# Kernel tuning notes

Measured on AMD Instinct MI355X. Metric: run time of the kernel, lower is better.

## Reference

```python
import jax, jax.numpy as jnp
import numpy as np

N_NODES = 100000
N_EDGES = 1600000
IN_FEATS = 128
OUT_FEATS = 128
LN_EPS = 1e-5


def setup_inputs() -> dict:
    key = jax.random.key(0)
    k_h, k_w, k_b, k_src, k_dst = jax.random.split(key, 5)
    stdv = 1.0 / np.sqrt(OUT_FEATS)
    return {
        "h": jax.random.normal(k_h, (N_NODES, IN_FEATS), dtype=jnp.float32),
        "weight": jax.random.uniform(k_w, (IN_FEATS, OUT_FEATS), dtype=jnp.float32, minval=-stdv, maxval=stdv),
        "bias": jax.random.uniform(k_b, (OUT_FEATS,), dtype=jnp.float32, minval=-stdv, maxval=stdv),
        "gamma": jnp.ones((OUT_FEATS,), dtype=jnp.float32),
        "beta": jnp.zeros((OUT_FEATS,), dtype=jnp.float32),
        "src": jax.random.randint(k_src, (N_EDGES,), 0, N_NODES, dtype=jnp.int32),
        "dst": jax.random.randint(k_dst, (N_EDGES,), 0, N_NODES, dtype=jnp.int32),
    }


def reference(h, weight, bias, gamma, beta, src, dst):
    n = h.shape[0]
    # in-degree norm: 1/deg with inf -> 0 (isolated nodes)
    deg = jax.ops.segment_sum(jnp.ones_like(dst, dtype=h.dtype), dst, num_segments=n)
    norm = jnp.where(deg > 0, 1.0 / deg, 0.0)[:, None]  # [N, 1]
    # update_all(copy_src, sum): scatter-add of source features onto destinations
    ah = jax.ops.segment_sum(h[src], dst, num_segments=n)  # [N, in_feats]
    x = ah * norm
    x = x @ weight + bias  # [N, out_feats]
    # LayerNorm over feature dim with affine params
    mu = jnp.mean(x, axis=-1, keepdims=True)
    var = jnp.mean(jnp.square(x - mu), axis=-1, keepdims=True)
    x = (x - mu) * jax.lax.rsqrt(var + LN_EPS) * gamma + beta
    return jax.nn.relu(x)
```

## Files before the change

kernel.cpp:

```cpp
#include <hip/hip_runtime.h>

#define F 128
#define SCANB 1024
#define NBLK 128
#define BSHIFT 6
#define MAXNB 4096
#define SMEM_BYTES 43264

typedef __attribute__((ext_vector_type(8))) short short8;
typedef __attribute__((ext_vector_type(4))) float f32x4;

static __device__ __forceinline__ short f2bf(float f) {
    union { float f; unsigned u; } v; v.f = f;
    unsigned r = v.u + 0x7FFF + ((v.u >> 16) & 1);
    return (short)(r >> 16);
}
static __device__ __forceinline__ float bf_lo(unsigned u) {
    return __builtin_bit_cast(float, u << 16);
}
static __device__ __forceinline__ float bf_hi(unsigned u) {
    return __builtin_bit_cast(float, u & 0xFFFF0000u);
}
static __device__ __forceinline__ uint4 pack8(float a0,float a1,float a2,float a3,
                                              float a4,float a5,float a6,float a7) {
    uint4 o;
    o.x = ((unsigned)(unsigned short)f2bf(a1) << 16) | (unsigned short)f2bf(a0);
    o.y = ((unsigned)(unsigned short)f2bf(a3) << 16) | (unsigned short)f2bf(a2);
    o.z = ((unsigned)(unsigned short)f2bf(a5) << 16) | (unsigned short)f2bf(a4);
    o.w = ((unsigned)(unsigned short)f2bf(a7) << 16) | (unsigned short)f2bf(a6);
    return o;
}

__global__ __launch_bounds__(256) void k_gemm_hist(
    const float* __restrict__ h, const float* __restrict__ w,
    unsigned* __restrict__ hb, const int* __restrict__ dst,
    int* __restrict__ mat, int n_nodes, int n_edges, int nb, int hblk) {
    __shared__ alignas(16) char smem[SMEM_BYTES];
    const int tid = threadIdx.x;
    const int bid = blockIdx.x;

    if (bid < hblk) {
        int* lh = (int*)smem;
        for (int i = tid; i < nb; i += 256) lh[i] = 0;
        __syncthreads();
        const int epb = (n_edges + hblk - 1) / hblk;
        const int e0 = bid * epb, e1 = min(e0 + epb, n_edges);
        for (int e = e0 + tid; e < e1; e += 256)
            atomicAdd(&lh[dst[e] >> BSHIFT], 1);
        __syncthreads();
        for (int i = tid; i < nb; i += 256)
            mat[(size_t)i * NBLK + bid] = lh[i];
        return;
    }

    short* wt = (short*)smem;
    float* xs = (float*)(smem + 34816);
    {
        int n = tid & 127;
        for (int k = tid >> 7; k < 128; k += 2)
            wt[n * 136 + k] = f2bf(w[(size_t)k * 128 + n]);
    }
    __syncthreads();

    const int wv = tid >> 6, l = tid & 63, lr = l & 15, lk = l >> 4, q = l & 15;
    const int base = (bid - hblk) * 64;
    if (base >= n_nodes) return;
    const int row = base + wv * 16 + lr;
    const bool valid = row < n_nodes;

    short8 af[4];
    #pragma unroll
    for (int kk = 0; kk < 4; ++kk) {
        int k0 = kk * 32 + lk * 8;
        float4 a0{0,0,0,0}, a1{0,0,0,0};
        if (valid) {
            a0 = *(const float4*)(h + (size_t)row * F + k0);
            a1 = *(const float4*)(h + (size_t)row * F + k0 + 4);
        }
        af[kk] = short8{ f2bf(a0.x), f2bf(a0.y), f2bf(a0.z), f2bf(a0.w),
                         f2bf(a1.x), f2bf(a1.y), f2bf(a1.z), f2bf(a1.w) };
    }
    f32x4 acc[8];
    #pragma unroll
    for (int n = 0; n < 8; ++n) acc[n] = f32x4{0, 0, 0, 0};
    #pragma unroll
    for (int kk = 0; kk < 4; ++kk) {
        const int kb = kk * 32 + lk * 8;
        #pragma unroll
        for (int n = 0; n < 8; ++n) {
            short8 bfr = *(const short8*)(&wt[(n * 16 + lr) * 136 + kb]);
            acc[n] = __builtin_amdgcn_mfma_f32_16x16x32_bf16(af[kk], bfr, acc[n], 0, 0, 0);
        }
    }
    float* xw = xs + wv * (4 * 132);
    #pragma unroll
    for (int r = 0; r < 4; ++r) {
        #pragma unroll
        for (int n = 0; n < 8; ++n)
            xw[lk * 132 + n * 16 + lr] = acc[n][r];
        int grow = base + wv * 16 + lk * 4 + r;
        float4 a = *(const float4*)&xw[lk * 132 + q * 8];
        float4 b = *(const float4*)&xw[lk * 132 + q * 8 + 4];
        uint4 o = pack8(a.x, a.y, a.z, a.w, b.x, b.y, b.z, b.w);
        if (grow < n_nodes)
            ((uint4*)hb)[(size_t)grow * 16 + q] = o;
    }
}

__global__ __launch_bounds__(SCANB) void k_scan_a(const int* in, int* out,
                                                  int* bsum, int n) {
    __shared__ int tmp[SCANB];
    int i = blockIdx.x * SCANB + threadIdx.x;
    int v = (i < n) ? in[i] : 0;
    tmp[threadIdx.x] = v;
    __syncthreads();
    for (int off = 1; off < SCANB; off <<= 1) {
        int t = (threadIdx.x >= off) ? tmp[threadIdx.x - off] : 0;
        __syncthreads();
        tmp[threadIdx.x] += t;
        __syncthreads();
    }
    if (i < n) out[i] = tmp[threadIdx.x] - v;
    if (threadIdx.x == SCANB - 1) bsum[blockIdx.x] = tmp[SCANB - 1];
}

__global__ __launch_bounds__(512) void k_scan_b(int* bsum, int nb) {
    __shared__ int tmp[512];
    int i = threadIdx.x;
    int v = (i < nb) ? bsum[i] : 0;
    tmp[i] = v;
    __syncthreads();
    for (int off = 1; off < 512; off <<= 1) {
        int t = (i >= off) ? tmp[i - off] : 0;
        __syncthreads();
        tmp[i] += t;
        __syncthreads();
    }
    if (i < nb) bsum[i] = tmp[i] - v;
}

__global__ __launch_bounds__(SCANB) void k_scan_c(int* out, const int* bsum, int n) {
    int i = blockIdx.x * SCANB + threadIdx.x;
    if (i < n) out[i] += bsum[blockIdx.x];
}

__global__ __launch_bounds__(256) void k_part_scatter(
    const int* __restrict__ src, const int* __restrict__ dst,
    const int* __restrict__ mat, const int* __restrict__ bsum,
    unsigned* __restrict__ binned, int n_edges, int nb, int epb) {
    __shared__ int lbase[MAXNB];
    const int bid = blockIdx.x;
    for (int i = threadIdx.x; i < nb; i += 256) {
        int idx = i * NBLK + bid;
        lbase[i] = mat[idx] + bsum[idx >> 10];
    }
    __syncthreads();
    int e0 = bid * epb;
    int e1 = min(e0 + epb, n_edges);
    for (int e = e0 + threadIdx.x; e < e1; e += 256) {
        int d = dst[e];
        int b = d >> BSHIFT;
        int pos = atomicAdd(&lbase[b], 1);
        binned[pos] = ((unsigned)(d & ((1 << BSHIFT) - 1)) << 26) | (unsigned)src[e];
    }
}

__global__ __launch_bounds__(256) void k_bin_to_csr(
    const unsigned* __restrict__ binned, const int* __restrict__ mat,
    const int* __restrict__ bsum, int* __restrict__ deg, int* __restrict__ offs,
    int* __restrict__ esrc, int n_edges, int n_nodes, int nb) {
    __shared__ int ldeg[64], loffs[64], lcur[64];
    int b = blockIdx.x;
    int i0 = b * NBLK;
    int start = mat[i0] + bsum[i0 >> 10];
    int end = n_edges;
    if (b + 1 < nb) {
        int i1 = (b + 1) * NBLK;
        end = mat[i1] + bsum[i1 >> 10];
    }
    int cnt = end - start;
    int base_node = b << BSHIFT;
    int nn = min(1 << BSHIFT, n_nodes - base_node);
    for (int i = threadIdx.x; i < nn; i += 256) { ldeg[i] = 0; lcur[i] = 0; }
    __syncthreads();
    for (int i = threadIdx.x; i < cnt; i += 256)
        atomicAdd(&ldeg[binned[start + i] >> 26], 1);
    __syncthreads();
    if (threadIdx.x == 0) {
        int run = 0;
        for (int i = 0; i < nn; ++i) { loffs[i] = run; run += ldeg[i]; }
    }
    __syncthreads();
    for (int i = threadIdx.x; i < nn; i += 256) {
        deg[base_node + i]  = ldeg[i];
        offs[base_node + i] = start + loffs[i];
    }
    for (int i = threadIdx.x; i < cnt; i += 256) {
        unsigned p = binned[start + i];
        int ln = p >> 26;
        int pos = start + loffs[ln] + atomicAdd(&lcur[ln], 1);
        esrc[pos] = (int)(p & ((1u << 26) - 1));
    }
}

__global__ __launch_bounds__(256) void k_hist(const int* __restrict__ dst,
                                              int* __restrict__ deg, int n_edges) {
    int e = blockIdx.x * 256 + threadIdx.x;
    if (e < n_edges) atomicAdd(&deg[dst[e]], 1);
}

__global__ __launch_bounds__(256) void k_scatter_idx(
    const int* __restrict__ src, const int* __restrict__ dst,
    const int* __restrict__ offs, int* __restrict__ cursor,
    int* __restrict__ esrc, int n_edges) {
    int e = blockIdx.x * 256 + threadIdx.x;
    if (e >= n_edges) return;
    int d = dst[e];
    int pos = offs[d] + atomicAdd(&cursor[d], 1);
    esrc[pos] = src[e];
}

__global__ __launch_bounds__(256) void k_gather_ln(
    const unsigned* __restrict__ hb, const int* __restrict__ esrc,
    const int* __restrict__ offs, const int* __restrict__ deg,
    const float* __restrict__ bias, const float* __restrict__ gamma,
    const float* __restrict__ beta, float* __restrict__ out, int n_nodes) {
    int t = blockIdx.x * 256 + threadIdx.x;
    int node = t >> 6;
    int l = t & 63;
    if (node >= n_nodes) return;
    const int g = l >> 4;
    const int q = l & 15;

    float4 bs0 = *(const float4*)(bias  + q * 8);
    float4 bs1 = *(const float4*)(bias  + q * 8 + 4);
    float4 gm0 = *(const float4*)(gamma + q * 8);
    float4 gm1 = *(const float4*)(gamma + q * 8 + 4);
    float4 bt0 = *(const float4*)(beta  + q * 8);
    float4 bt1 = *(const float4*)(beta  + q * 8 + 4);

    const int start = offs[node];
    const int dn = deg[node];
    const int end = start + dn;

    float a0=0,a1=0,a2=0,a3=0,a4=0,a5=0,a6=0,a7=0;
    int i = start;
    for (; i + 8 <= end; i += 8) {
        int s0 = esrc[i + g];
        int s1 = esrc[i + 4 + g];
        uint4 v0 = *((const uint4*)(hb + (size_t)s0 * 64 + q * 4));
        uint4 v1 = *((const uint4*)(hb + (size_t)s1 * 64 + q * 4));
        a0 += bf_lo(v0.x) + bf_lo(v1.x); a1 += bf_hi(v0.x) + bf_hi(v1.x);
        a2 += bf_lo(v0.y) + bf_lo(v1.y); a3 += bf_hi(v0.y) + bf_hi(v1.y);
        a4 += bf_lo(v0.z) + bf_lo(v1.z); a5 += bf_hi(v0.z) + bf_hi(v1.z);
        a6 += bf_lo(v0.w) + bf_lo(v1.w); a7 += bf_hi(v0.w) + bf_hi(v1.w);
    }
    for (; i < end; i += 4) {
        int e = i + g;
        if (e < end) {
            int s = esrc[e];
            uint4 v = *((const uint4*)(hb + (size_t)s * 64 + q * 4));
            a0 += bf_lo(v.x); a1 += bf_hi(v.x);
            a2 += bf_lo(v.y); a3 += bf_hi(v.y);
            a4 += bf_lo(v.z); a5 += bf_hi(v.z);
            a6 += bf_lo(v.w); a7 += bf_hi(v.w);
        }
    }
    #pragma unroll
    for (int m = 16; m <= 32; m <<= 1) {
        a0 += __shfl_xor(a0, m); a1 += __shfl_xor(a1, m);
        a2 += __shfl_xor(a2, m); a3 += __shfl_xor(a3, m);
        a4 += __shfl_xor(a4, m); a5 += __shfl_xor(a5, m);
        a6 += __shfl_xor(a6, m); a7 += __shfl_xor(a7, m);
    }
    const float nv = dn > 0 ? 1.0f / (float)dn : 0.0f;
    float f0 = a0 * nv + bs0.x, f1 = a1 * nv + bs0.y;
    float f2 = a2 * nv + bs0.z, f3 = a3 * nv + bs0.w;
    float f4 = a4 * nv + bs1.x, f5 = a5 * nv + bs1.y;
    float f6 = a6 * nv + bs1.z, f7 = a7 * nv + bs1.w;

    float s  = ((f0 + f1) + (f2 + f3)) + ((f4 + f5) + (f6 + f7));
    float q2 = ((f0*f0 + f1*f1) + (f2*f2 + f3*f3)) + ((f4*f4 + f5*f5) + (f6*f6 + f7*f7));
    #pragma unroll
    for (int m = 1; m <= 8; m <<= 1) {
        s  += __shfl_xor(s, m);
        q2 += __shfl_xor(q2, m);
    }
    float mu   = s * (1.0f / F);
    float var  = q2 * (1.0f / F) - mu * mu;
    float rstd = rsqrtf(var + 1e-5f);

    if (g == 0) {
        float4 o0, o1;
        o0.x = fmaxf((f0 - mu) * rstd * gm0.x + bt0.x, 0.0f);
        o0.y = fmaxf((f1 - mu) * rstd * gm0.y + bt0.y, 0.0f);
        o0.z = fmaxf((f2 - mu) * rstd * gm0.z + bt0.z, 0.0f);
        o0.w = fmaxf((f3 - mu) * rstd * gm0.w + bt0.w, 0.0f);
        o1.x = fmaxf((f4 - mu) * rstd * gm1.x + bt1.x, 0.0f);
        o1.y = fmaxf((f5 - mu) * rstd * gm1.y + bt1.y, 0.0f);
        o1.z = fmaxf((f6 - mu) * rstd * gm1.z + bt1.z, 0.0f);
        o1.w = fmaxf((f7 - mu) * rstd * gm1.w + bt1.w, 0.0f);
        float* op = out + (size_t)node * F + q * 8;
        *(float4*)op = o0;
        *(float4*)(op + 4) = o1;
    }
}

extern "C" void kernel_launch(void* const* d_in, const int* in_sizes, int n_in,
                              void* d_out, int out_size, void* d_ws, size_t ws_size,
                              hipStream_t stream) {
    const float* h      = (const float*)d_in[0];
    const float* weight = (const float*)d_in[1];
    const float* bias   = (const float*)d_in[2];
    const float* gamma  = (const float*)d_in[3];
    const float* beta   = (const float*)d_in[4];
    const int*   src    = (const int*)d_in[5];
    const int*   dst    = (const int*)d_in[6];

    const int n_nodes = in_sizes[0] / F;
    const int n_edges = in_sizes[5];

    float* x = (float*)d_out;

    const int nb = (n_nodes + (1 << BSHIFT) - 1) >> BSHIFT;
    const int len = nb * NBLK;
    const int nscan = (len + SCANB - 1) / SCANB;
    const bool shift_ok = (nb <= MAXNB) && (nscan <= 512) && (n_nodes <= (1 << 26));

    int* deg    = (int*)d_ws;
    int* offs   = deg + n_nodes;
    int* esrc   = offs + n_nodes;
    unsigned* hb = (unsigned*)(esrc + n_edges);
    int* bsum   = (int*)(hb + (size_t)n_nodes * 64);
    int* mat    = bsum + 1024;
    unsigned* binned = (unsigned*)(mat + (size_t)len);
    int* cursor = mat;

    size_t need_common = ((size_t)2 * n_nodes + (size_t)n_edges + 1024) * sizeof(int)
                       + (size_t)n_nodes * 64 * sizeof(unsigned);
    size_t need_new  = need_common + ((size_t)len + (size_t)n_edges) * sizeof(int);
    size_t need_fall = need_common + (size_t)n_nodes * sizeof(int);
    bool use_new = shift_ok && ws_size >= need_new;

    const int gb = (n_nodes + 63) / 64;

    if (use_new) {
        k_gemm_hist<<<NBLK + gb, 256, 0, stream>>>(h, weight, hb, dst, mat,
                                                   n_nodes, n_edges, nb, NBLK);
        k_scan_a<<<nscan, SCANB, 0, stream>>>(mat, mat, bsum, len);
        k_scan_b<<<1, 512, 0, stream>>>(bsum, nscan);
        const int epb = (n_edges + NBLK - 1) / NBLK;
        k_part_scatter<<<NBLK, 256, 0, stream>>>(src, dst, mat, bsum, binned,
                                                 n_edges, nb, epb);
        k_bin_to_csr<<<nb, 256, 0, stream>>>(binned, mat, bsum, deg, offs, esrc,
                                             n_edges, n_nodes, nb);
    } else if (ws_size >= need_fall) {
        k_gemm_hist<<<gb, 256, 0, stream>>>(h, weight, hb, dst, mat,
                                            n_nodes, n_edges, nb, 0);
        const int nscan2 = (n_nodes + SCANB - 1) / SCANB;
        hipMemsetAsync(deg, 0, (size_t)n_nodes * sizeof(int), stream);
        hipMemsetAsync(cursor, 0, (size_t)n_nodes * sizeof(int), stream);
        k_hist<<<(n_edges + 255) / 256, 256, 0, stream>>>(dst, deg, n_edges);
        k_scan_a<<<nscan2, SCANB, 0, stream>>>(deg, offs, bsum, n_nodes);
        k_scan_b<<<1, 512, 0, stream>>>(bsum, nscan2);
        k_scan_c<<<nscan2, SCANB, 0, stream>>>(offs, bsum, n_nodes);
        k_scatter_idx<<<(n_edges + 255) / 256, 256, 0, stream>>>(
            src, dst, offs, cursor, esrc, n_edges);
    }

    int gblocks = (int)(((size_t)n_nodes * 64 + 255) / 256);
    k_gather_ln<<<gblocks, 256, 0, stream>>>(hb, esrc, offs, deg,
                                             bias, gamma, beta, x, n_nodes);
}
```

Measured before the change: 144.8 us.

## Fuse bin-to-CSR conversion with gather, normalization and LayerNorm per bin

```diff
diff --git a/kernel.cpp b/kernel.cpp
--- a/kernel.cpp
+++ b/kernel.cpp
@@ -5,6 +5,7 @@
 #define NBLK 128
 #define BSHIFT 6
 #define MAXNB 4096
+#define CAP 4096
 #define SMEM_BYTES 43264
 
 typedef __attribute__((ext_vector_type(8))) short short8;
@@ -165,41 +166,134 @@
     }
 }
 
-__global__ __launch_bounds__(256) void k_bin_to_csr(
+__global__ __launch_bounds__(256) void k_csr_gather(
     const unsigned* __restrict__ binned, const int* __restrict__ mat,
-    const int* __restrict__ bsum, int* __restrict__ deg, int* __restrict__ offs,
-    int* __restrict__ esrc, int n_edges, int n_nodes, int nb) {
+    const int* __restrict__ bsum, const unsigned* __restrict__ hb,
+    const float* __restrict__ bias, const float* __restrict__ gamma,
+    const float* __restrict__ beta, int* __restrict__ esrc,
+    float* __restrict__ out, int n_edges, int n_nodes, int nb) {
     __shared__ int ldeg[64], loffs[64], lcur[64];
-    int b = blockIdx.x;
-    int i0 = b * NBLK;
-    int start = mat[i0] + bsum[i0 >> 10];
+    __shared__ int lesrc[CAP];
+
+    const int tid = threadIdx.x;
+    const int b = blockIdx.x;
+    const int i0 = b * NBLK;
+    const int start = mat[i0] + bsum[i0 >> 10];
     int end = n_edges;
     if (b + 1 < nb) {
         int i1 = (b + 1) * NBLK;
         end = mat[i1] + bsum[i1 >> 10];
     }
-    int cnt = end - start;
-    int base_node = b << BSHIFT;
-    int nn = min(1 << BSHIFT, n_nodes - base_node);
-    for (int i = threadIdx.x; i < nn; i += 256) { ldeg[i] = 0; lcur[i] = 0; }
-    __syncthreads();
-    for (int i = threadIdx.x; i < cnt; i += 256)
+    const int cnt = end - start;
+    const int base_node = b << BSHIFT;
+    const int nn = min(1 << BSHIFT, n_nodes - base_node);
+
+    for (int i = tid; i < 64; i += 256) { ldeg[i] = 0; lcur[i] = 0; }
+    __syncthreads();
+    for (int i = tid; i < cnt; i += 256)
         atomicAdd(&ldeg[binned[start + i] >> 26], 1);
     __syncthreads();
-    if (threadIdx.x == 0) {
+    if (tid == 0) {
         int run = 0;
         for (int i = 0; i < nn; ++i) { loffs[i] = run; run += ldeg[i]; }
     }
     __syncthreads();
-    for (int i = threadIdx.x; i < nn; i += 256) {
-        deg[base_node + i]  = ldeg[i];
-        offs[base_node + i] = start + loffs[i];
-    }
-    for (int i = threadIdx.x; i < cnt; i += 256) {
-        unsigned p = binned[start + i];
-        int ln = p >> 26;
-        int pos = start + loffs[ln] + atomicAdd(&lcur[ln], 1);
-        esrc[pos] = (int)(p & ((1u << 26) - 1));
+
+    const bool inLds = cnt <= CAP;
+    if (inLds) {
+        for (int i = tid; i < cnt; i += 256) {
+            unsigned p = binned[start + i];
+            int ln = p >> 26;
+            int pos = loffs[ln] + atomicAdd(&lcur[ln], 1);
+            lesrc[pos] = (int)(p & ((1u << 26) - 1));
+        }
+    } else {
+        for (int i = tid; i < cnt; i += 256) {
+            unsigned p = binned[start + i];
+            int ln = p >> 26;
+            int pos = loffs[ln] + atomicAdd(&lcur[ln], 1);
+            esrc[start + pos] = (int)(p & ((1u << 26) - 1));
+        }
+    }
+    __syncthreads();
+
+    const int wv = tid >> 6, l = tid & 63, g = l >> 4, q = l & 15;
+    const int* ep = inLds ? (const int*)lesrc : (const int*)(esrc + start);
+
+    float4 bs0 = *(const float4*)(bias  + q * 8);
+    float4 bs1 = *(const float4*)(bias  + q * 8 + 4);
+    float4 gm0 = *(const float4*)(gamma + q * 8);
+    float4 gm1 = *(const float4*)(gamma + q * 8 + 4);
+    float4 bt0 = *(const float4*)(beta  + q * 8);
+    float4 bt1 = *(const float4*)(beta  + q * 8 + 4);
+
+    for (int ni = 0; ni < 16; ++ni) {
+        int ln = wv * 16 + ni;
+        if (ln >= nn) break;
+        const int eb = loffs[ln];
+        const int dn = ldeg[ln];
+
+        float a0=0,a1=0,a2=0,a3=0,a4=0,a5=0,a6=0,a7=0;
+        int i = 0;
+        for (; i + 8 <= dn; i += 8) {
+            int s0 = ep[eb + i + g];
+            int s1 = ep[eb + i + 4 + g];
+            uint4 v0 = *((const uint4*)(hb + (size_t)s0 * 64 + q * 4));
+            uint4 v1 = *((const uint4*)(hb + (size_t)s1 * 64 + q * 4));
+            a0 += bf_lo(v0.x) + bf_lo(v1.x); a1 += bf_hi(v0.x) + bf_hi(v1.x);
+            a2 += bf_lo(v0.y) + bf_lo(v1.y); a3 += bf_hi(v0.y) + bf_hi(v1.y);
+            a4 += bf_lo(v0.z) + bf_lo(v1.z); a5 += bf_hi(v0.z) + bf_hi(v1.z);
+            a6 += bf_lo(v0.w) + bf_lo(v1.w); a7 += bf_hi(v0.w) + bf_hi(v1.w);
+        }
+        for (; i < dn; i += 4) {
+            int e = i + g;
+            if (e < dn) {
+                int s = ep[eb + e];
+                uint4 v = *((const uint4*)(hb + (size_t)s * 64 + q * 4));
+                a0 += bf_lo(v.x); a1 += bf_hi(v.x);
+                a2 += bf_lo(v.y); a3 += bf_hi(v.y);
+                a4 += bf_lo(v.z); a5 += bf_hi(v.z);
+                a6 += bf_lo(v.w); a7 += bf_hi(v.w);
+            }
+        }
+        #pragma unroll
+        for (int m = 16; m <= 32; m <<= 1) {
+            a0 += __shfl_xor(a0, m); a1 += __shfl_xor(a1, m);
+            a2 += __shfl_xor(a2, m); a3 += __shfl_xor(a3, m);
+            a4 += __shfl_xor(a4, m); a5 += __shfl_xor(a5, m);
+            a6 += __shfl_xor(a6, m); a7 += __shfl_xor(a7, m);
+        }
+        const float nv = dn > 0 ? 1.0f / (float)dn : 0.0f;
+        float f0 = a0 * nv + bs0.x, f1 = a1 * nv + bs0.y;
+        float f2 = a2 * nv + bs0.z, f3 = a3 * nv + bs0.w;
+        float f4 = a4 * nv + bs1.x, f5 = a5 * nv + bs1.y;
+        float f6 = a6 * nv + bs1.z, f7 = a7 * nv + bs1.w;
+
+        float s  = ((f0 + f1) + (f2 + f3)) + ((f4 + f5) + (f6 + f7));
+        float q2 = ((f0*f0 + f1*f1) + (f2*f2 + f3*f3)) + ((f4*f4 + f5*f5) + (f6*f6 + f7*f7));
+        #pragma unroll
+        for (int m = 1; m <= 8; m <<= 1) {
+            s  += __shfl_xor(s, m);
+            q2 += __shfl_xor(q2, m);
+        }
+        float mu   = s * (1.0f / F);
+        float var  = q2 * (1.0f / F) - mu * mu;
+        float rstd = rsqrtf(var + 1e-5f);
+
+        if (g == 0) {
+            float4 o0, o1;
+            o0.x = fmaxf((f0 - mu) * rstd * gm0.x + bt0.x, 0.0f);
+            o0.y = fmaxf((f1 - mu) * rstd * gm0.y + bt0.y, 0.0f);
+            o0.z = fmaxf((f2 - mu) * rstd * gm0.z + bt0.z, 0.0f);
+            o0.w = fmaxf((f3 - mu) * rstd * gm0.w + bt0.w, 0.0f);
+            o1.x = fmaxf((f4 - mu) * rstd * gm1.x + bt1.x, 0.0f);
+            o1.y = fmaxf((f5 - mu) * rstd * gm1.y + bt1.y, 0.0f);
+            o1.z = fmaxf((f6 - mu) * rstd * gm1.z + bt1.z, 0.0f);
+            o1.w = fmaxf((f7 - mu) * rstd * gm1.w + bt1.w, 0.0f);
+            float* op = out + (size_t)(base_node + ln) * F + q * 8;
+            *(float4*)op = o0;
+            *(float4*)(op + 4) = o1;
+        }
     }
 }
 
@@ -352,7 +446,8 @@
         const int epb = (n_edges + NBLK - 1) / NBLK;
         k_part_scatter<<<NBLK, 256, 0, stream>>>(src, dst, mat, bsum, binned,
                                                  n_edges, nb, epb);
-        k_bin_to_csr<<<nb, 256, 0, stream>>>(binned, mat, bsum, deg, offs, esrc,
+        k_csr_gather<<<nb, 256, 0, stream>>>(binned, mat, bsum, hb,
+                                             bias, gamma, beta, esrc, x,
                                              n_edges, n_nodes, nb);
     } else if (ws_size >= need_fall) {
         k_gemm_hist<<<gb, 256, 0, stream>>>(h, weight, hb, dst, mat,
@@ -366,9 +461,8 @@
         k_scan_c<<<nscan2, SCANB, 0, stream>>>(offs, bsum, n_nodes);
         k_scatter_idx<<<(n_edges + 255) / 256, 256, 0, stream>>>(
             src, dst, offs, cursor, esrc, n_edges);
-    }
-
-    int gblocks = (int)(((size_t)n_nodes * 64 + 255) / 256);
-    k_gather_ln<<<gblocks, 256, 0, stream>>>(hb, esrc, offs, deg,
-                                             bias, gamma, beta, x, n_nodes);
-}
+        int gblocks = (int)(((size_t)n_nodes * 64 + 255) / 256);
+        k_gather_ln<<<gblocks, 256, 0, stream>>>(hb, esrc, offs, deg,
+                                                 bias, gamma, beta, x, n_nodes);
+    }
+}
```

Result: slower. 155.9 us (+7.7%).

## Split GEMM tiles across histogram and scatter kernels; unroll gather by 16

Applied to the files above, without the earlier changes.

```diff
diff --git a/kernel.cpp b/kernel.cpp
--- a/kernel.cpp
+++ b/kernel.cpp
@@ -31,28 +31,9 @@
     return o;
 }
 
-__global__ __launch_bounds__(256) void k_gemm_hist(
+static __device__ __forceinline__ void gemm_tile(
     const float* __restrict__ h, const float* __restrict__ w,
-    unsigned* __restrict__ hb, const int* __restrict__ dst,
-    int* __restrict__ mat, int n_nodes, int n_edges, int nb, int hblk) {
-    __shared__ alignas(16) char smem[SMEM_BYTES];
-    const int tid = threadIdx.x;
-    const int bid = blockIdx.x;
-
-    if (bid < hblk) {
-        int* lh = (int*)smem;
-        for (int i = tid; i < nb; i += 256) lh[i] = 0;
-        __syncthreads();
-        const int epb = (n_edges + hblk - 1) / hblk;
-        const int e0 = bid * epb, e1 = min(e0 + epb, n_edges);
-        for (int e = e0 + tid; e < e1; e += 256)
-            atomicAdd(&lh[dst[e] >> BSHIFT], 1);
-        __syncthreads();
-        for (int i = tid; i < nb; i += 256)
-            mat[(size_t)i * NBLK + bid] = lh[i];
-        return;
-    }
-
+    unsigned* __restrict__ hb, int n_nodes, int base, char* smem, int tid) {
     short* wt = (short*)smem;
     float* xs = (float*)(smem + 34816);
     {
@@ -63,7 +44,6 @@
     __syncthreads();
 
     const int wv = tid >> 6, l = tid & 63, lr = l & 15, lk = l >> 4, q = l & 15;
-    const int base = (bid - hblk) * 64;
     if (base >= n_nodes) return;
     const int row = base + wv * 16 + lr;
     const bool valid = row < n_nodes;
@@ -107,6 +87,60 @@
     }
 }
 
+__global__ __launch_bounds__(256) void k_gemm_hist(
+    const float* __restrict__ h, const float* __restrict__ w,
+    unsigned* __restrict__ hb, const int* __restrict__ dst,
+    int* __restrict__ mat, int n_nodes, int n_edges, int nb, int hblk) {
+    __shared__ alignas(16) char smem[SMEM_BYTES];
+    const int tid = threadIdx.x;
+    const int bid = blockIdx.x;
+
+    if (bid < hblk) {
+        int* lh = (int*)smem;
+        for (int i = tid; i < nb; i += 256) lh[i] = 0;
+        __syncthreads();
+        const int epb = (n_edges + hblk - 1) / hblk;
+        const int e0 = bid * epb, e1 = min(e0 + epb, n_edges);
+        for (int e = e0 + tid; e < e1; e += 256)
+            atomicAdd(&lh[dst[e] >> BSHIFT], 1);
+        __syncthreads();
+        for (int i = tid; i < nb; i += 256)
+            mat[(size_t)i * NBLK + bid] = lh[i];
+        return;
+    }
+    gemm_tile(h, w, hb, n_nodes, (bid - hblk) * 64, smem, tid);
+}
+
+__global__ __launch_bounds__(256) void k_scatter_gemm(
+    const int* __restrict__ src, const int* __restrict__ dst,
+    const int* __restrict__ mat, const int* __restrict__ bsum,
+    unsigned* __restrict__ binned, int n_edges, int nb, int epb,
+    const float* __restrict__ h, const float* __restrict__ w,
+    unsigned* __restrict__ hb, int n_nodes, int row0) {
+    __shared__ alignas(16) char smem[SMEM_BYTES];
+    const int tid = threadIdx.x;
+    const int bid = blockIdx.x;
+
+    if (bid < NBLK) {
+        int* lbase = (int*)smem;
+        for (int i = tid; i < nb; i += 256) {
+            int idx = i * NBLK + bid;
+            lbase[i] = mat[idx] + bsum[idx >> 10];
+        }
+        __syncthreads();
+        int e0 = bid * epb;
+        int e1 = min(e0 + epb, n_edges);
+        for (int e = e0 + tid; e < e1; e += 256) {
+            int d = dst[e];
+            int b = d >> BSHIFT;
+            int pos = atomicAdd(&lbase[b], 1);
+            binned[pos] = ((unsigned)(d & ((1 << BSHIFT) - 1)) << 26) | (unsigned)src[e];
+        }
+        return;
+    }
+    gemm_tile(h, w, hb, n_nodes, row0 + (bid - NBLK) * 64, smem, tid);
+}
+
 __global__ __launch_bounds__(SCANB) void k_scan_a(const int* in, int* out,
                                                   int* bsum, int n) {
     __shared__ int tmp[SCANB];
@@ -142,27 +176,6 @@
 __global__ __launch_bounds__(SCANB) void k_scan_c(int* out, const int* bsum, int n) {
     int i = blockIdx.x * SCANB + threadIdx.x;
     if (i < n) out[i] += bsum[blockIdx.x];
-}
-
-__global__ __launch_bounds__(256) void k_part_scatter(
-    const int* __restrict__ src, const int* __restrict__ dst,
-    const int* __restrict__ mat, const int* __restrict__ bsum,
-    unsigned* __restrict__ binned, int n_edges, int nb, int epb) {
-    __shared__ int lbase[MAXNB];
-    const int bid = blockIdx.x;
-    for (int i = threadIdx.x; i < nb; i += 256) {
-        int idx = i * NBLK + bid;
-        lbase[i] = mat[idx] + bsum[idx >> 10];
-    }
-    __syncthreads();
-    int e0 = bid * epb;
-    int e1 = min(e0 + epb, n_edges);
-    for (int e = e0 + threadIdx.x; e < e1; e += 256) {
-        int d = dst[e];
-        int b = d >> BSHIFT;
-        int pos = atomicAdd(&lbase[b], 1);
-        binned[pos] = ((unsigned)(d & ((1 << BSHIFT) - 1)) << 26) | (unsigned)src[e];
-    }
 }
 
 __global__ __launch_bounds__(256) void k_bin_to_csr(
@@ -232,19 +245,30 @@
     const int g = l >> 4;
     const int q = l & 15;
 
-    float4 bs0 = *(const float4*)(bias  + q * 8);
-    float4 bs1 = *(const float4*)(bias  + q * 8 + 4);
-    float4 gm0 = *(const float4*)(gamma + q * 8);
-    float4 gm1 = *(const float4*)(gamma + q * 8 + 4);
-    float4 bt0 = *(const float4*)(beta  + q * 8);
-    float4 bt1 = *(const float4*)(beta  + q * 8 + 4);
-
     const int start = offs[node];
     const int dn = deg[node];
     const int end = start + dn;
 
     float a0=0,a1=0,a2=0,a3=0,a4=0,a5=0,a6=0,a7=0;
     int i = start;
+    for (; i + 16 <= end; i += 16) {
+        int s0 = esrc[i + g];
+        int s1 = esrc[i + 4 + g];
+        int s2 = esrc[i + 8 + g];
+        int s3 = esrc[i + 12 + g];
+        uint4 v0 = *((const uint4*)(hb + (size_t)s0 * 64 + q * 4));
+        uint4 v1 = *((const uint4*)(hb + (size_t)s1 * 64 + q * 4));
+        uint4 v2 = *((const uint4*)(hb + (size_t)s2 * 64 + q * 4));
+        uint4 v3 = *((const uint4*)(hb + (size_t)s3 * 64 + q * 4));
+        a0 += (bf_lo(v0.x) + bf_lo(v1.x)) + (bf_lo(v2.x) + bf_lo(v3.x));
+        a1 += (bf_hi(v0.x) + bf_hi(v1.x)) + (bf_hi(v2.x) + bf_hi(v3.x));
+        a2 += (bf_lo(v0.y) + bf_lo(v1.y)) + (bf_lo(v2.y) + bf_lo(v3.y));
+        a3 += (bf_hi(v0.y) + bf_hi(v1.y)) + (bf_hi(v2.y) + bf_hi(v3.y));
+        a4 += (bf_lo(v0.z) + bf_lo(v1.z)) + (bf_lo(v2.z) + bf_lo(v3.z));
+        a5 += (bf_hi(v0.z) + bf_hi(v1.z)) + (bf_hi(v2.z) + bf_hi(v3.z));
+        a6 += (bf_lo(v0.w) + bf_lo(v1.w)) + (bf_lo(v2.w) + bf_lo(v3.w));
+        a7 += (bf_hi(v0.w) + bf_hi(v1.w)) + (bf_hi(v2.w) + bf_hi(v3.w));
+    }
     for (; i + 8 <= end; i += 8) {
         int s0 = esrc[i + g];
         int s1 = esrc[i + 4 + g];
@@ -273,6 +297,8 @@
         a4 += __shfl_xor(a4, m); a5 += __shfl_xor(a5, m);
         a6 += __shfl_xor(a6, m); a7 += __shfl_xor(a7, m);
     }
+    float4 bs0 = *(const float4*)(bias  + q * 8);
+    float4 bs1 = *(const float4*)(bias  + q * 8 + 4);
     const float nv = dn > 0 ? 1.0f / (float)dn : 0.0f;
     float f0 = a0 * nv + bs0.x, f1 = a1 * nv + bs0.y;
     float f2 = a2 * nv + bs0.z, f3 = a3 * nv + bs0.w;
@@ -291,6 +317,10 @@
     float rstd = rsqrtf(var + 1e-5f);
 
     if (g == 0) {
+        float4 gm0 = *(const float4*)(gamma + q * 8);
+        float4 gm1 = *(const float4*)(gamma + q * 8 + 4);
+        float4 bt0 = *(const float4*)(beta  + q * 8);
+        float4 bt1 = *(const float4*)(beta  + q * 8 + 4);
         float4 o0, o1;
         o0.x = fmaxf((f0 - mu) * rstd * gm0.x + bt0.x, 0.0f);
         o0.y = fmaxf((f1 - mu) * rstd * gm0.y + bt0.y, 0.0f);
@@ -345,15 +375,21 @@
     const int gb = (n_nodes + 63) / 64;
 
     if (use_new) {
-        k_gemm_hist<<<NBLK + gb, 256, 0, stream>>>(h, weight, hb, dst, mat,
+        const int g1 = gb / 2;
+        const int g2 = gb - g1;
+        k_gemm_hist<<<NBLK + g1, 256, 0, stream>>>(h, weight, hb, dst, mat,
                                                    n_nodes, n_edges, nb, NBLK);
         k_scan_a<<<nscan, SCANB, 0, stream>>>(mat, mat, bsum, len);
         k_scan_b<<<1, 512, 0, stream>>>(bsum, nscan);
         const int epb = (n_edges + NBLK - 1) / NBLK;
-        k_part_scatter<<<NBLK, 256, 0, stream>>>(src, dst, mat, bsum, binned,
-                                                 n_edges, nb, epb);
+        k_scatter_gemm<<<NBLK + g2, 256, 0, stream>>>(src, dst, mat, bsum, binned,
+                                                      n_edges, nb, epb,
+                                                      h, weight, hb, n_nodes, g1 * 64);
         k_bin_to_csr<<<nb, 256, 0, stream>>>(binned, mat, bsum, deg, offs, esrc,
                                              n_edges, n_nodes, nb);
+        int gblocks = (int)(((size_t)n_nodes * 64 + 255) / 256);
+        k_gather_ln<<<gblocks, 256, 0, stream>>>(hb, esrc, offs, deg,
+                                                 bias, gamma, beta, x, n_nodes);
     } else if (ws_size >= need_fall) {
         k_gemm_hist<<<gb, 256, 0, stream>>>(h, weight, hb, dst, mat,
                                             n_nodes, n_edges, nb, 0);
@@ -366,9 +402,8 @@
         k_scan_c<<<nscan2, SCANB, 0, stream>>>(offs, bsum, n_nodes);
         k_scatter_idx<<<(n_edges + 255) / 256, 256, 0, stream>>>(
             src, dst, offs, cursor, esrc, n_edges);
-    }
-
-    int gblocks = (int)(((size_t)n_nodes * 64 + 255) / 256);
-    k_gather_ln<<<gblocks, 256, 0, stream>>>(hb, esrc, offs, deg,
-                                             bias, gamma, beta, x, n_nodes);
-}
+        int gblocks = (int)(((size_t)n_nodes * 64 + 255) / 256);
+        k_gather_ln<<<gblocks, 256, 0, stream>>>(hb, esrc, offs, deg,
+                                                 bias, gamma, beta, x, n_nodes);
+    }
+}
```

New measurement: 144.5 us. No clear change (-0.2%).
